# Kernel tuning notes

Hardware: AMD Instinct MI355X
Metric: run time of the kernel (lower is better)

## Reference

```python
import jax, jax.numpy as jnp
import numpy as np
from jax import lax


def fake_quant_w(w):
    # Brevitas Int8WeightPerTensorFloat-style: per-tensor symmetric int8 fake quant
    scale = jnp.max(jnp.abs(w)) / 127.0
    wq = jnp.clip(jnp.round(w / scale), -128.0, 127.0) * scale
    return w + lax.stop_gradient(wq - w)


def conv(x, w, b, groups):
    y = lax.conv_general_dilated(
        x, w,
        window_strides=(1, 1),
        padding='SAME' if w.shape[-1] == 3 else 'VALID',
        dimension_numbers=('NCHW', 'OIHW', 'NCHW'),
        feature_group_count=groups,
    )
    return y + b[None, :, None, None]


def setup_inputs() -> dict:
    key = jax.random.key(0)
    ks = jax.random.split(key, 9)
    B, C_in, C_hid, H, W = 16, 128, 256, 64, 128
    x = jax.random.normal(ks[0], (B, C_in, H, W), dtype=jnp.float32)
    # depthwise conv1: groups=C_in, OIHW = [C_in, 1, 3, 3]
    dw1 = jax.random.normal(ks[1], (C_in, 1, 3, 3), dtype=jnp.float32) * 0.1
    db1 = jax.random.normal(ks[2], (C_in,), dtype=jnp.float32) * 0.01
    # pointwise conv1: [C_hid, C_in, 1, 1]
    pw1 = jax.random.normal(ks[3], (C_hid, C_in, 1, 1), dtype=jnp.float32) * 0.05
    pb1 = jax.random.normal(ks[4], (C_hid,), dtype=jnp.float32) * 0.01
    # depthwise conv2: [C_hid, 1, 3, 3]
    dw2 = jax.random.normal(ks[5], (C_hid, 1, 3, 3), dtype=jnp.float32) * 0.1
    db2 = jax.random.normal(ks[6], (C_hid,), dtype=jnp.float32) * 0.01
    # pointwise conv2: [2, C_hid, 1, 1]
    pw2 = jax.random.normal(ks[7], (2, C_hid, 1, 1), dtype=jnp.float32) * 0.05
    pb2 = jax.random.normal(ks[8], (2,), dtype=jnp.float32) * 0.01
    return {'x': x, 'dw1': dw1, 'db1': db1, 'pw1': pw1, 'pb1': pb1,
            'dw2': dw2, 'db2': db2, 'pw2': pw2, 'pb2': pb2}


def reference(x, dw1, db1, pw1, pb1, dw2, db2, pw2, pb2):
    C_in = x.shape[1]
    C_hid = pw1.shape[0]
    h = conv(x, fake_quant_w(dw1), db1, groups=C_in)      # depthwise 3x3
    h = conv(h, fake_quant_w(pw1), pb1, groups=1)          # pointwise -> C_hid
    h = jax.nn.relu(h)
    h = conv(h, fake_quant_w(dw2), db2, groups=C_hid)      # depthwise 3x3
    out = conv(h, fake_quant_w(pw2), pb2, groups=1)        # pointwise -> 2
    return out
```

## Files before the change

### kernel.cpp

```cpp
#include <hip/hip_runtime.h>
#include <math.h>

#define C_IN  128
#define C_HID 256
#define HGT   64
#define WID   128
#define NBATCH 16
#define HW (HGT * WID)

typedef unsigned int   uint32;
typedef unsigned short u16;
typedef float f32x4  __attribute__((ext_vector_type(4)));
typedef short bf16x8 __attribute__((ext_vector_type(8)));

__device__ __forceinline__ uint32 f2bf_bits(float f) {
    uint32 u = __float_as_uint(f);
    u = (u + 0x7fff + ((u >> 16) & 1)) >> 16;
    return u;
}
__device__ __forceinline__ float qclip(float v) {
    return fminf(fmaxf(v, -128.0f), 127.0f);
}

__global__ __launch_bounds__(1024) void quant4_kernel(
    const float* __restrict__ dw1, const float* __restrict__ pw1,
    const float* __restrict__ dw2, const float* __restrict__ pw2,
    const float* __restrict__ db2,
    float* __restrict__ qdw1T, u16* __restrict__ Blin,
    u16* __restrict__ W18lin, float* __restrict__ scales)
{
    const float* w; int n;
    switch (blockIdx.x) {
        case 0:  w = dw1; n = C_IN * 9;    break;
        case 1:  w = pw1; n = C_HID * C_IN; break;
        case 2:  w = dw2; n = C_HID * 9;   break;
        default: w = pw2; n = 2 * C_HID;   break;
    }
    __shared__ float sm[1024];
    int tid = threadIdx.x;
    const f32x4* w4 = (const f32x4*)w;
    int n4 = n >> 2;
    float m = 0.0f;
    #pragma unroll 4
    for (int i = tid; i < n4; i += 1024) {
        f32x4 v = w4[i];
        m = fmaxf(m, fmaxf(fmaxf(fabsf(v.x), fabsf(v.y)),
                           fmaxf(fabsf(v.z), fabsf(v.w))));
    }
    sm[tid] = m;
    __syncthreads();
    for (int s = 512; s > 0; s >>= 1) {
        if (tid < s) sm[tid] = fmaxf(sm[tid], sm[tid + s]);
        __syncthreads();
    }
    const float scale = sm[0] / 127.0f;

    if (blockIdx.x == 0) {
        for (int i = tid; i < C_IN * 9; i += 1024) {
            int t = i >> 7, cin = i & 127;
            float v = qclip(rintf(dw1[cin * 9 + t] / scale));
            qdw1T[i] = v * scale;
        }
    } else if (blockIdx.x == 1) {
        if (tid == 0) scales[0] = scale;
        #pragma unroll
        for (int i = tid; i < 4096; i += 1024) {
            int kstep = i >> 10;
            int cf    = (i >> 6) & 15;
            int l     = i & 63;
            int co    = cf * 16 + (l & 15);
            int k0    = kstep * 32 + ((l >> 4) << 3);
            const float* src = pw1 + (size_t)co * C_IN + k0;
            f32x4 a = *(const f32x4*)src;
            f32x4 b = *(const f32x4*)(src + 4);
            float vv[8] = {a.x, a.y, a.z, a.w, b.x, b.y, b.z, b.w};
            uint32 pk[4];
            #pragma unroll
            for (int p = 0; p < 4; ++p) {
                float v0 = qclip(rintf(vv[2 * p]     / scale));
                float v1 = qclip(rintf(vv[2 * p + 1] / scale));
                pk[p] = f2bf_bits(v0) | (f2bf_bits(v1) << 16);
            }
            ((uint4*)Blin)[i] = make_uint4(pk[0], pk[1], pk[2], pk[3]);
        }
    } else if (blockIdx.x == 2) {
    } else {
        const float s_p = scale;
        __syncthreads();

        const f32x4* d4 = (const f32x4*)dw2;
        float md = 0.0f;
        for (int i = tid; i < 576; i += 1024) {
            f32x4 v = d4[i];
            md = fmaxf(md, fmaxf(fmaxf(fabsf(v.x), fabsf(v.y)),
                                 fmaxf(fabsf(v.z), fabsf(v.w))));
        }
        sm[tid] = md;
        __syncthreads();
        for (int s = 512; s > 0; s >>= 1) {
            if (tid < s) sm[tid] = fmaxf(sm[tid], sm[tid + s]);
            __syncthreads();
        }
        const float s_d = sm[0] / 127.0f;

        {
            int ks  = tid >> 7;
            int jt  = (tid >> 6) & 1;
            int l   = tid & 63;
            int j   = jt * 16 + (l & 15);
            int ch0 = ks * 32 + ((l >> 4) << 3);
            uint32 pk[4] = {0, 0, 0, 0};
            if (j < 18) {
                int t9 = j >> 1, o = j & 1;
                float wv[8];
                #pragma unroll
                for (int p = 0; p < 8; ++p) {
                    int ch = ch0 + p;
                    float qd = qclip(rintf(dw2[ch * 9 + t9] / s_d)) * s_d;
                    float qp = qclip(rintf(pw2[o * C_HID + ch] / s_p)) * s_p;
                    wv[p] = qd * qp;
                }
                #pragma unroll
                for (int p = 0; p < 4; ++p)
                    pk[p] = f2bf_bits(wv[2 * p]) | (f2bf_bits(wv[2 * p + 1]) << 16);
            }
            ((uint4*)W18lin)[tid] = make_uint4(pk[0], pk[1], pk[2], pk[3]);
        }

        #pragma unroll
        for (int o = 0; o < 2; ++o) {
            __syncthreads();
            if (tid < 256) {
                float qv = qclip(rintf(pw2[o * C_HID + tid] / s_p)) * s_p;
                sm[tid] = qv * db2[tid];
            }
            __syncthreads();
            for (int s = 128; s > 0; s >>= 1) {
                if (tid < s) sm[tid] += sm[tid + s];
                __syncthreads();
            }
            if (tid == 0) scales[1 + o] = sm[0];
        }
    }
}

__global__ __launch_bounds__(512, 4) void fused_main(
    const float* __restrict__ x,
    const float* __restrict__ qdw1T, const float* __restrict__ db1,
    const u16* __restrict__ Blin, const float* __restrict__ pb1,
    const u16* __restrict__ W18lin,
    const float* __restrict__ scales,
    float* __restrict__ Pg)
{
    __shared__ __align__(16) unsigned char smem_raw[C_HID * 132 * 2];
    __shared__ float Ml[128][20];
    u16 (*h1s)[136]  = (u16 (*)[136])smem_raw;
    u16 (*h2pm)[264] = (u16 (*)[264])smem_raw;

    const int bid = blockIdx.x;
    const int swz = (bid & 7) * 128 + (bid >> 3);
    const int nb  = swz >> 6;
    const int y   = swz & 63;
    const int tid = threadIdx.x;
    const int wave = tid >> 6, lane = tid & 63;

    {
        const int q = tid & 31, g = tid >> 5;
        const int px0 = q << 2, cin0 = g << 3;

        f32x4 bia = *(const f32x4*)(db1 + cin0);
        f32x4 bib = *(const f32x4*)(db1 + cin0 + 4);
        float a32[8][4];
        #pragma unroll
        for (int c = 0; c < 8; ++c) {
            float b = (c < 4) ? ((const float*)&bia)[c] : ((const float*)&bib)[c - 4];
            #pragma unroll
            for (int p = 0; p < 4; ++p) a32[c][p] = b;
        }

        #pragma unroll
        for (int ky = 0; ky < 3; ++ky) {
            int yy = y + ky - 1;
            if (yy < 0 || yy >= HGT) continue;
            const float* xbase = x + (((size_t)nb * C_IN + cin0) * HGT + yy) * WID;

            f32x4 mid[8];
            #pragma unroll
            for (int c = 0; c < 8; ++c)
                mid[c] = *(const f32x4*)(xbase + (size_t)c * HW + px0);

            float w3[3][8];
            #pragma unroll
            for (int kx = 0; kx < 3; ++kx) {
                f32x4 wa = *(const f32x4*)(qdw1T + (ky * 3 + kx) * C_IN + cin0);
                f32x4 wb = *(const f32x4*)(qdw1T + (ky * 3 + kx) * C_IN + cin0 + 4);
                w3[kx][0] = wa.x; w3[kx][1] = wa.y; w3[kx][2] = wa.z; w3[kx][3] = wa.w;
                w3[kx][4] = wb.x; w3[kx][5] = wb.y; w3[kx][6] = wb.z; w3[kx][7] = wb.w;
            }

            #pragma unroll
            for (int c = 0; c < 8; ++c) {
                float lf = __shfl_up(mid[c].w, 1);
                float rt = __shfl_down(mid[c].x, 1);
                lf = (q > 0)  ? lf : 0.0f;
                rt = (q < 31) ? rt : 0.0f;
                float seg[6] = {lf, mid[c].x, mid[c].y, mid[c].z, mid[c].w, rt};
                #pragma unroll
                for (int kx = 0; kx < 3; ++kx)
                    #pragma unroll
                    for (int p = 0; p < 4; ++p)
                        a32[c][p] = fmaf(w3[kx][c], seg[p + kx], a32[c][p]);
            }
        }

        #pragma unroll
        for (int p = 0; p < 4; ++p) {
            uint32 pk[4];
            #pragma unroll
            for (int i = 0; i < 4; ++i)
                pk[i] = f2bf_bits(a32[2 * i][p]) | (f2bf_bits(a32[2 * i + 1][p]) << 16);
            *(uint4*)&h1s[px0 + p][cin0] = make_uint4(pk[0], pk[1], pk[2], pk[3]);
        }
    }
    __syncthreads();

    const int l15 = lane & 15, l4 = lane >> 4;
    const int wco = wave >> 2;
    const int wpx = wave & 3;
    const int px0w = wpx << 5;
    const float bscale = scales[0];

    f32x4 acc[2][8];
    #pragma unroll
    for (int f = 0; f < 2; ++f)
        #pragma unroll
        for (int c = 0; c < 8; ++c) acc[f][c] = f32x4{0, 0, 0, 0};

    const bf16x8* BL = (const bf16x8*)Blin;

    #pragma unroll
    for (int ks = 0; ks < 4; ++ks) {
        bf16x8 bfrag[8];
        #pragma unroll
        for (int c = 0; c < 8; ++c)
            bfrag[c] = BL[(ks * 16 + wco * 8 + c) * 64 + lane];
        bf16x8 afrag[2];
        #pragma unroll
        for (int f = 0; f < 2; ++f)
            afrag[f] = *(const bf16x8*)&h1s[px0w + f * 16 + l15][ks * 32 + l4 * 8];
        #pragma unroll
        for (int f = 0; f < 2; ++f)
            #pragma unroll
            for (int c = 0; c < 8; ++c)
                acc[f][c] = __builtin_amdgcn_mfma_f32_16x16x32_bf16(
                    afrag[f], bfrag[c], acc[f][c], 0, 0, 0);
    }

    __syncthreads();

    #pragma unroll
    for (int f = 0; f < 2; ++f) {
        int pxb = px0w + f * 16 + l4 * 4;
        #pragma unroll
        for (int c = 0; c < 8; ++c) {
            int co = wco * 128 + c * 16 + l15;
            float bias = pb1[co];
            float v0 = fmaxf(fmaf(acc[f][c].x, bscale, bias), 0.0f);
            float v1 = fmaxf(fmaf(acc[f][c].y, bscale, bias), 0.0f);
            float v2 = fmaxf(fmaf(acc[f][c].z, bscale, bias), 0.0f);
            float v3 = fmaxf(fmaf(acc[f][c].w, bscale, bias), 0.0f);
            h2pm[pxb + 0][co] = (u16)f2bf_bits(v0);
            h2pm[pxb + 1][co] = (u16)f2bf_bits(v1);
            h2pm[pxb + 2][co] = (u16)f2bf_bits(v2);
            h2pm[pxb + 3][co] = (u16)f2bf_bits(v3);
        }
    }
    __syncthreads();

    {
        const int px0t = wave << 4;
        const bf16x8* WL = (const bf16x8*)W18lin;

        f32x4 acc2[2];
        acc2[0] = f32x4{0, 0, 0, 0};
        acc2[1] = f32x4{0, 0, 0, 0};

        #pragma unroll 2
        for (int ks = 0; ks < 8; ++ks) {
            bf16x8 af = *(const bf16x8*)&h2pm[px0t + l15][ks * 32 + l4 * 8];
            bf16x8 b0 = WL[(ks * 2 + 0) * 64 + lane];
            bf16x8 b1 = WL[(ks * 2 + 1) * 64 + lane];
            acc2[0] = __builtin_amdgcn_mfma_f32_16x16x32_bf16(af, b0, acc2[0], 0, 0, 0);
            acc2[1] = __builtin_amdgcn_mfma_f32_16x16x32_bf16(af, b1, acc2[1], 0, 0, 0);
        }

        #pragma unroll
        for (int i = 0; i < 4; ++i)
            Ml[px0t + l4 * 4 + i][l15] = acc2[0][i];
        if (l15 < 2) {
            #pragma unroll
            for (int i = 0; i < 4; ++i)
                Ml[px0t + l4 * 4 + i][16 + l15] = acc2[1][i];
        }
    }
    __syncthreads();

    for (int t = tid; t < 768; t += 512) {
        int r = t >> 7, px = t & 127;
        int ky = r >> 1, o = r & 1;
        float v = 0.0f;
        #pragma unroll
        for (int kx = 0; kx < 3; ++kx) {
            int pxs = px + kx - 1;
            if (pxs >= 0 && pxs < WID)
                v += Ml[pxs][(ky * 3 + kx) * 2 + o];
        }
        Pg[((size_t)(nb * HGT + y) * 6 + r) * WID + px] = v;
    }
}

__global__ __launch_bounds__(512) void gather_out(
    const float* __restrict__ Pg, const float* __restrict__ pb2,
    const float* __restrict__ scales, float* __restrict__ out)
{
    int idx = blockIdx.x * 512 + threadIdx.x;
    int px = idx & 127;
    int yy = (idx >> 7) & 63;
    int o  = (idx >> 13) & 1;
    int nb = idx >> 14;
    float v = pb2[o] + scales[1 + o];
    #pragma unroll
    for (int ky = 0; ky < 3; ++ky) {
        int z = yy + ky - 1;
        if (z >= 0 && z < HGT)
            v += Pg[((size_t)(nb * HGT + z) * 6 + ky * 2 + o) * WID + px];
    }
    out[idx] = v;
}

extern "C" void kernel_launch(void* const* d_in, const int* in_sizes, int n_in,
                              void* d_out, int out_size, void* d_ws, size_t ws_size,
                              hipStream_t stream) {
    const float* x   = (const float*)d_in[0];
    const float* dw1 = (const float*)d_in[1];
    const float* db1 = (const float*)d_in[2];
    const float* pw1 = (const float*)d_in[3];
    const float* pb1 = (const float*)d_in[4];
    const float* dw2 = (const float*)d_in[5];
    const float* db2 = (const float*)d_in[6];
    const float* pw2 = (const float*)d_in[7];
    const float* pb2 = (const float*)d_in[8];
    float* out = (float*)d_out;

    char* wsb = (char*)d_ws;
    u16*   Blin   = (u16*)wsb;
    float* qdw1T  = (float*)(wsb + 65536);
    float* scales = (float*)(wsb + 65536 + 4608);
    u16*   W18lin = (u16*)(wsb + 65536 + 4608 + 64);
    float* Pg     = (float*)(wsb + 98304);

    quant4_kernel<<<4, 1024, 0, stream>>>(dw1, pw1, dw2, pw2, db2,
                                          qdw1T, Blin, W18lin, scales);

    fused_main<<<NBATCH * HGT, 512, 0, stream>>>(
        x, qdw1T, db1, Blin, pb1, W18lin, scales, Pg);

    gather_out<<<512, 512, 0, stream>>>(Pg, pb2, scales, out);
}
```

Measured before the change: 48.40 us.

## Split fused block per row into two 64-pixel halves, move horizontal taps to gather

Each block now handles half of an image row (64 pixels), which doubles the grid to 2048 blocks. Per-thread work shrinks (4 channels instead of 8, one MFMA pixel tile instead of two), and LDS use drops to raise occupancy. Halo pixels at the half boundary are read straight from global memory. The horizontal 3-tap combine of the second depthwise conv moves from fused_main into gather_out. The intermediate buffer grows from 6 to 18 values per pixel, so global write and read traffic goes up, and the gather kernel does 9 loads per output instead of 3.

After: 56.81 us. 1.17x slower.

```diff
diff --git a/kernel.cpp b/kernel.cpp
--- a/kernel.cpp
+++ b/kernel.cpp
@@ -150,60 +150,58 @@
     const u16* __restrict__ Blin, const float* __restrict__ pb1,
     const u16* __restrict__ W18lin,
     const float* __restrict__ scales,
-    float* __restrict__ Pg)
+    float* __restrict__ Mg)
 {
-    __shared__ __align__(16) unsigned char smem_raw[C_HID * 132 * 2];
-    __shared__ float Ml[128][20];
-    u16 (*h1s)[136]  = (u16 (*)[136])smem_raw;
+    __shared__ __align__(16) unsigned char smem_raw[64 * 264 * 2];
+    __shared__ float Ml[18][66];
+    u16 (*h1s)[140]  = (u16 (*)[140])smem_raw;
     u16 (*h2pm)[264] = (u16 (*)[264])smem_raw;
 
     const int bid = blockIdx.x;
-    const int swz = (bid & 7) * 128 + (bid >> 3);
-    const int nb  = swz >> 6;
-    const int y   = swz & 63;
+    const int swz = (bid & 7) * 256 + (bid >> 3);
+    const int nb  = swz >> 7;
+    const int y   = (swz >> 1) & 63;
+    const int xh  = swz & 1;
+    const int pxb0 = xh << 6;
     const int tid = threadIdx.x;
     const int wave = tid >> 6, lane = tid & 63;
 
     {
-        const int q = tid & 31, g = tid >> 5;
-        const int px0 = q << 2, cin0 = g << 3;
+        const int q = tid & 15, g = tid >> 4;
+        const int px0 = q << 2, cin0 = g << 2;
 
         f32x4 bia = *(const f32x4*)(db1 + cin0);
-        f32x4 bib = *(const f32x4*)(db1 + cin0 + 4);
-        float a32[8][4];
-        #pragma unroll
-        for (int c = 0; c < 8; ++c) {
-            float b = (c < 4) ? ((const float*)&bia)[c] : ((const float*)&bib)[c - 4];
-            #pragma unroll
-            for (int p = 0; p < 4; ++p) a32[c][p] = b;
-        }
+        float a32[4][4];
+        #pragma unroll
+        for (int c = 0; c < 4; ++c)
+            #pragma unroll
+            for (int p = 0; p < 4; ++p) a32[c][p] = ((const float*)&bia)[c];
 
         #pragma unroll
         for (int ky = 0; ky < 3; ++ky) {
             int yy = y + ky - 1;
             if (yy < 0 || yy >= HGT) continue;
-            const float* xbase = x + (((size_t)nb * C_IN + cin0) * HGT + yy) * WID;
-
-            f32x4 mid[8];
-            #pragma unroll
-            for (int c = 0; c < 8; ++c)
-                mid[c] = *(const f32x4*)(xbase + (size_t)c * HW + px0);
-
-            float w3[3][8];
+            const float* rowbase = x + (((size_t)nb * C_IN + cin0) * HGT + yy) * WID + pxb0;
+
+            f32x4 mid[4];
+            #pragma unroll
+            for (int c = 0; c < 4; ++c)
+                mid[c] = *(const f32x4*)(rowbase + (size_t)c * HW + px0);
+
+            float w3[3][4];
             #pragma unroll
             for (int kx = 0; kx < 3; ++kx) {
-                f32x4 wa = *(const f32x4*)(qdw1T + (ky * 3 + kx) * C_IN + cin0);
-                f32x4 wb = *(const f32x4*)(qdw1T + (ky * 3 + kx) * C_IN + cin0 + 4);
-                w3[kx][0] = wa.x; w3[kx][1] = wa.y; w3[kx][2] = wa.z; w3[kx][3] = wa.w;
-                w3[kx][4] = wb.x; w3[kx][5] = wb.y; w3[kx][6] = wb.z; w3[kx][7] = wb.w;
-            }
-
-            #pragma unroll
-            for (int c = 0; c < 8; ++c) {
+                f32x4 wv = *(const f32x4*)(qdw1T + (ky * 3 + kx) * C_IN + cin0);
+                w3[kx][0] = wv.x; w3[kx][1] = wv.y; w3[kx][2] = wv.z; w3[kx][3] = wv.w;
+            }
+
+            #pragma unroll
+            for (int c = 0; c < 4; ++c) {
+                const float* rowc = rowbase + (size_t)c * HW;
                 float lf = __shfl_up(mid[c].w, 1);
                 float rt = __shfl_down(mid[c].x, 1);
-                lf = (q > 0)  ? lf : 0.0f;
-                rt = (q < 31) ? rt : 0.0f;
+                if (q == 0)  lf = xh        ? rowc[px0 - 1] : 0.0f;
+                if (q == 15) rt = (xh == 0) ? rowc[px0 + 4] : 0.0f;
                 float seg[6] = {lf, mid[c].x, mid[c].y, mid[c].z, mid[c].w, rt};
                 #pragma unroll
                 for (int kx = 0; kx < 3; ++kx)
@@ -215,112 +213,83 @@
 
         #pragma unroll
         for (int p = 0; p < 4; ++p) {
-            uint32 pk[4];
-            #pragma unroll
-            for (int i = 0; i < 4; ++i)
-                pk[i] = f2bf_bits(a32[2 * i][p]) | (f2bf_bits(a32[2 * i + 1][p]) << 16);
-            *(uint4*)&h1s[px0 + p][cin0] = make_uint4(pk[0], pk[1], pk[2], pk[3]);
+            uint2 pk;
+            pk.x = f2bf_bits(a32[0][p]) | (f2bf_bits(a32[1][p]) << 16);
+            pk.y = f2bf_bits(a32[2][p]) | (f2bf_bits(a32[3][p]) << 16);
+            *(uint2*)&h1s[px0 + p][cin0] = pk;
         }
     }
     __syncthreads();
 
     const int l15 = lane & 15, l4 = lane >> 4;
-    const int wco = wave >> 2;
-    const int wpx = wave & 3;
-    const int px0w = wpx << 5;
+    const int pxt = wave & 3;
+    const int coh = wave >> 2;
+    const int px0w = pxt << 4;
     const float bscale = scales[0];
 
-    f32x4 acc[2][8];
+    f32x4 acc[8];
     #pragma unroll
-    for (int f = 0; f < 2; ++f)
-        #pragma unroll
-        for (int c = 0; c < 8; ++c) acc[f][c] = f32x4{0, 0, 0, 0};
+    for (int c = 0; c < 8; ++c) acc[c] = f32x4{0, 0, 0, 0};
 
     const bf16x8* BL = (const bf16x8*)Blin;
 
     #pragma unroll
     for (int ks = 0; ks < 4; ++ks) {
-        bf16x8 bfrag[8];
-        #pragma unroll
-        for (int c = 0; c < 8; ++c)
-            bfrag[c] = BL[(ks * 16 + wco * 8 + c) * 64 + lane];
-        bf16x8 afrag[2];
-        #pragma unroll
-        for (int f = 0; f < 2; ++f)
-            afrag[f] = *(const bf16x8*)&h1s[px0w + f * 16 + l15][ks * 32 + l4 * 8];
-        #pragma unroll
-        for (int f = 0; f < 2; ++f)
-            #pragma unroll
-            for (int c = 0; c < 8; ++c)
-                acc[f][c] = __builtin_amdgcn_mfma_f32_16x16x32_bf16(
-                    afrag[f], bfrag[c], acc[f][c], 0, 0, 0);
+        bf16x8 afrag = *(const bf16x8*)&h1s[px0w + l15][ks * 32 + l4 * 8];
+        #pragma unroll
+        for (int c = 0; c < 8; ++c) {
+            bf16x8 bfrag = BL[(ks * 16 + coh * 8 + c) * 64 + lane];
+            acc[c] = __builtin_amdgcn_mfma_f32_16x16x32_bf16(afrag, bfrag, acc[c], 0, 0, 0);
+        }
     }
 
     __syncthreads();
 
     #pragma unroll
-    for (int f = 0; f < 2; ++f) {
-        int pxb = px0w + f * 16 + l4 * 4;
-        #pragma unroll
-        for (int c = 0; c < 8; ++c) {
-            int co = wco * 128 + c * 16 + l15;
-            float bias = pb1[co];
-            float v0 = fmaxf(fmaf(acc[f][c].x, bscale, bias), 0.0f);
-            float v1 = fmaxf(fmaf(acc[f][c].y, bscale, bias), 0.0f);
-            float v2 = fmaxf(fmaf(acc[f][c].z, bscale, bias), 0.0f);
-            float v3 = fmaxf(fmaf(acc[f][c].w, bscale, bias), 0.0f);
-            h2pm[pxb + 0][co] = (u16)f2bf_bits(v0);
-            h2pm[pxb + 1][co] = (u16)f2bf_bits(v1);
-            h2pm[pxb + 2][co] = (u16)f2bf_bits(v2);
-            h2pm[pxb + 3][co] = (u16)f2bf_bits(v3);
+    for (int c = 0; c < 8; ++c) {
+        int co = coh * 128 + c * 16 + l15;
+        int pxb = px0w + l4 * 4;
+        float bias = pb1[co];
+        #pragma unroll
+        for (int i = 0; i < 4; ++i) {
+            float v = fmaxf(fmaf(acc[c][i], bscale, bias), 0.0f);
+            h2pm[pxb + i][co] = (u16)f2bf_bits(v);
         }
     }
     __syncthreads();
 
     {
-        const int px0t = wave << 4;
+        const int pxt3 = wave & 3;
+        const int jt   = wave >> 2;
+        const int px0t = pxt3 << 4;
         const bf16x8* WL = (const bf16x8*)W18lin;
 
-        f32x4 acc2[2];
-        acc2[0] = f32x4{0, 0, 0, 0};
-        acc2[1] = f32x4{0, 0, 0, 0};
-
+        f32x4 acc2 = f32x4{0, 0, 0, 0};
         #pragma unroll 2
         for (int ks = 0; ks < 8; ++ks) {
             bf16x8 af = *(const bf16x8*)&h2pm[px0t + l15][ks * 32 + l4 * 8];
-            bf16x8 b0 = WL[(ks * 2 + 0) * 64 + lane];
-            bf16x8 b1 = WL[(ks * 2 + 1) * 64 + lane];
-            acc2[0] = __builtin_amdgcn_mfma_f32_16x16x32_bf16(af, b0, acc2[0], 0, 0, 0);
-            acc2[1] = __builtin_amdgcn_mfma_f32_16x16x32_bf16(af, b1, acc2[1], 0, 0, 0);
-        }
-
-        #pragma unroll
-        for (int i = 0; i < 4; ++i)
-            Ml[px0t + l4 * 4 + i][l15] = acc2[0][i];
-        if (l15 < 2) {
+            bf16x8 bf = WL[(ks * 2 + jt) * 64 + lane];
+            acc2 = __builtin_amdgcn_mfma_f32_16x16x32_bf16(af, bf, acc2, 0, 0, 0);
+        }
+
+        int j = jt * 16 + l15;
+        if (j < 18) {
             #pragma unroll
             for (int i = 0; i < 4; ++i)
-                Ml[px0t + l4 * 4 + i][16 + l15] = acc2[1][i];
-        }
-    }
-    __syncthreads();
-
-    for (int t = tid; t < 768; t += 512) {
-        int r = t >> 7, px = t & 127;
-        int ky = r >> 1, o = r & 1;
-        float v = 0.0f;
-        #pragma unroll
-        for (int kx = 0; kx < 3; ++kx) {
-            int pxs = px + kx - 1;
-            if (pxs >= 0 && pxs < WID)
-                v += Ml[pxs][(ky * 3 + kx) * 2 + o];
-        }
-        Pg[((size_t)(nb * HGT + y) * 6 + r) * WID + px] = v;
+                Ml[j][px0t + l4 * 4 + i] = acc2[i];
+        }
+    }
+    __syncthreads();
+
+    {
+        float* base = Mg + (size_t)swz * (18 * 64);
+        for (int t = tid; t < 18 * 64; t += 512)
+            base[t] = Ml[t >> 6][t & 63];
     }
 }
 
 __global__ __launch_bounds__(512) void gather_out(
-    const float* __restrict__ Pg, const float* __restrict__ pb2,
+    const float* __restrict__ Mg, const float* __restrict__ pb2,
     const float* __restrict__ scales, float* __restrict__ out)
 {
     int idx = blockIdx.x * 512 + threadIdx.x;
@@ -332,8 +301,15 @@
     #pragma unroll
     for (int ky = 0; ky < 3; ++ky) {
         int z = yy + ky - 1;
-        if (z >= 0 && z < HGT)
-            v += Pg[((size_t)(nb * HGT + z) * 6 + ky * 2 + o) * WID + px];
+        if (z < 0 || z >= HGT) continue;
+        #pragma unroll
+        for (int kx = 0; kx < 3; ++kx) {
+            int pxs = px + kx - 1;
+            if (pxs < 0 || pxs >= WID) continue;
+            int xh2 = pxs >> 6, px2 = pxs & 63;
+            int j = (ky * 3 + kx) * 2 + o;
+            v += Mg[((size_t)(((nb * 64 + z) << 1) + xh2) * 18 + j) * 64 + px2];
+        }
     }
     out[idx] = v;
 }
@@ -357,13 +333,13 @@
     float* qdw1T  = (float*)(wsb + 65536);
     float* scales = (float*)(wsb + 65536 + 4608);
     u16*   W18lin = (u16*)(wsb + 65536 + 4608 + 64);
-    float* Pg     = (float*)(wsb + 98304);
+    float* Mg     = (float*)(wsb + 98304);
 
     quant4_kernel<<<4, 1024, 0, stream>>>(dw1, pw1, dw2, pw2, db2,
                                           qdw1T, Blin, W18lin, scales);
 
-    fused_main<<<NBATCH * HGT, 512, 0, stream>>>(
-        x, qdw1T, db1, Blin, pb1, W18lin, scales, Pg);
-
-    gather_out<<<512, 512, 0, stream>>>(Pg, pb2, scales, out);
-}
+    fused_main<<<NBATCH * HGT * 2, 512, 0, stream>>>(
+        x, qdw1T, db1, Blin, pb1, W18lin, scales, Mg);
+
+    gather_out<<<512, 512, 0, stream>>>(Mg, pb2, scales, out);
+}
```
